# Kernel tuning notes

Measured on AMD Instinct MI355X. Metric: run time of the kernel, lower is better.

Reference implementation:

```python
import jax, jax.numpy as jnp
import numpy as np

BS = 1024
IN_DIM = 16 * 16      # final_dim[0]*final_dim[1]
HIDDEN = 3000
ITEM = 3              # item_number
STEPS = 30


def setup_inputs() -> dict:
    key = jax.random.key(0)
    ks = jax.random.split(key, 16)

    def xavier(k, shape):
        fan_in, fan_out = shape[1], shape[0]
        lim = np.sqrt(6.0 / (fan_in + fan_out))
        return jax.random.uniform(k, shape, jnp.float32, -lim, lim)

    return {
        "z": jax.random.normal(ks[0], (BS, 16, 16), jnp.float32),
        # join MLP: in->512->256->3000, ReLU after each
        "W1": xavier(ks[1], (512, IN_DIM)), "b1": jnp.zeros((512,), jnp.float32),
        "W2": xavier(ks[2], (256, 512)),    "b2": jnp.zeros((256,), jnp.float32),
        "W3": xavier(ks[3], (HIDDEN, 256)), "b3": jnp.zeros((HIDDEN,), jnp.float32),
        # GRUCell (torch layout: rows ordered r, z, n)
        "Wih": xavier(ks[4], (3 * HIDDEN, ITEM)),
        "bih": jnp.zeros((3 * HIDDEN,), jnp.float32),
        "Whh": xavier(ks[5], (3 * HIDDEN, HIDDEN)),
        "bhh": jnp.zeros((3 * HIDDEN,), jnp.float32),
        # output readout hidden -> item_number
        "Wo": xavier(ks[6], (ITEM, HIDDEN)), "bo": jnp.zeros((ITEM,), jnp.float32),
    }


def reference(z, W1, b1, W2, b2, W3, b3, Wih, bih, Whh, bhh, Wo, bo):
    bs = z.shape[0]
    zf = z.reshape(bs, -1)                                  # [bs, 256]
    h = jax.nn.relu(zf @ W1.T + b1)
    h = jax.nn.relu(h @ W2.T + b2)
    h = jax.nn.relu(h @ W3.T + b3)                          # [bs, 3000] initial hidden
    x0 = jnp.zeros((bs, ITEM), z.dtype)

    def step(carry, _):
        h, x = carry
        gi = x @ Wih.T + bih                                # [bs, 3H]
        gh = h @ Whh.T + bhh                                # [bs, 3H]
        i_r, i_z, i_n = jnp.split(gi, 3, axis=-1)
        h_r, h_z, h_n = jnp.split(gh, 3, axis=-1)
        r = jax.nn.sigmoid(i_r + h_r)
        u = jax.nn.sigmoid(i_z + h_z)
        n = jnp.tanh(i_n + r * h_n)
        h_new = (1.0 - u) * n + u * h
        x_new = h_new @ Wo.T + bo + x                       # residual waypoint add
        return (h_new, x_new), x_new

    (_, _), wp = jax.lax.scan(step, (h, x0), None, length=STEPS)
    return jnp.transpose(wp, (1, 0, 2))                      # [bs, STEPS, ITEM]
```

## Files before the change

kernel.cpp:

```cpp
#include <hip/hip_runtime.h>
#include <cstdint>
#include <cstddef>

#define HID 3000
#define HP  3072
#define NB  1024
#define BM  128
#define BN  64
#define KT  48
#define BUFSZ 53248

typedef _Float16 f16;
typedef _Float16 f16x8 __attribute__((ext_vector_type(8)));
typedef float    f32x4 __attribute__((ext_vector_type(4)));

__device__ __forceinline__ float sigf(float v)  { return 1.0f / (1.0f + __expf(-v)); }
__device__ __forceinline__ float tanhf_(float v){ return 2.0f / (1.0f + __expf(-2.0f * v)) - 1.0f; }

__device__ __forceinline__ void gload16(const void* g, void* l) {
    __builtin_amdgcn_global_load_lds((const __attribute__((address_space(1))) void*)g,
                                     (__attribute__((address_space(3))) void*)l, 16, 0, 0);
}

__global__ __launch_bounds__(256) void convert_whh(const float* __restrict__ whh,
                                                   f16* __restrict__ whh16)
{
    const int S32 = 3 * HP * (HP / 32);
    int t = blockIdx.x * 256 + threadIdx.x;
    if (t >= S32) return;
    const int c32 = (t % (HP / 32)) * 32;
    const int rr  = (t / (HP / 32)) % HP;
    const int g   = t / ((HP / 32) * HP);
    f16* dst = whh16 + ((size_t)g * HP + rr) * HP + c32;
    if (rr < HID && c32 + 32 <= HID) {
        const float* src = whh + (size_t)(g * HID + rr) * HID + c32;
#pragma unroll
        for (int u = 0; u < 4; ++u) {
            float4 lo = *reinterpret_cast<const float4*>(src + u * 8);
            float4 hi = *reinterpret_cast<const float4*>(src + u * 8 + 4);
            f16x8 v;
            v[0] = (f16)lo.x; v[1] = (f16)lo.y; v[2] = (f16)lo.z; v[3] = (f16)lo.w;
            v[4] = (f16)hi.x; v[5] = (f16)hi.y; v[6] = (f16)hi.z; v[7] = (f16)hi.w;
            *reinterpret_cast<f16x8*>(dst + u * 8) = v;
        }
    } else {
#pragma unroll
        for (int u = 0; u < 4; ++u) {
            f16x8 v;
#pragma unroll
            for (int k = 0; k < 8; ++k) {
                const int cc = c32 + u * 8 + k;
                v[k] = (rr < HID && cc < HID) ? (f16)whh[(size_t)(g * HID + rr) * HID + cc]
                                              : (f16)0.0f;
            }
            *reinterpret_cast<f16x8*>(dst + u * 8) = v;
        }
    }
}

__global__ __launch_bounds__(256) void convert_w3(const float* __restrict__ w,
                                                  f16* __restrict__ w16)
{
    int t = blockIdx.x * 256 + threadIdx.x;
    if (t >= HP * 32) return;
    int rr = t >> 5, c8 = (t & 31) * 8;
    f16x8 v;
    if (rr < HID) {
        const float* src = w + (size_t)rr * 256 + c8;
        float4 lo = *reinterpret_cast<const float4*>(src);
        float4 hi = *reinterpret_cast<const float4*>(src + 4);
        v[0] = (f16)lo.x; v[1] = (f16)lo.y; v[2] = (f16)lo.z; v[3] = (f16)lo.w;
        v[4] = (f16)hi.x; v[5] = (f16)hi.y; v[6] = (f16)hi.z; v[7] = (f16)hi.w;
    } else {
#pragma unroll
        for (int i = 0; i < 8; ++i) v[i] = (f16)0.0f;
    }
    *reinterpret_cast<f16x8*>(w16 + (size_t)rr * 256 + c8) = v;
}

__global__ __launch_bounds__(256) void mlp_layer(const float* __restrict__ A, int K, int N, int ldo,
                                                 const float* __restrict__ W,
                                                 const float* __restrict__ bias,
                                                 float* __restrict__ outf, f16* __restrict__ outh)
{
    __shared__ float sA[4 * 512];
    const int b0 = blockIdx.x * 4;
    for (int idx = threadIdx.x; idx < 4 * K; idx += 256)
        sA[idx] = A[(size_t)b0 * K + idx];
    __syncthreads();
    for (int n = threadIdx.x; n < ldo; n += 256) {
        float acc[4] = {0.f, 0.f, 0.f, 0.f};
        if (n < N) {
            const float4* wr = reinterpret_cast<const float4*>(W + (size_t)n * K);
            for (int kk = 0; kk < (K >> 2); ++kk) {
                float4 w = wr[kk];
#pragma unroll
                for (int r = 0; r < 4; ++r) {
                    const float* ar = sA + r * K + kk * 4;
                    acc[r] += ar[0] * w.x + ar[1] * w.y + ar[2] * w.z + ar[3] * w.w;
                }
            }
            float bv = bias[n];
#pragma unroll
            for (int r = 0; r < 4; ++r) acc[r] = fmaxf(acc[r] + bv, 0.f);
        }
#pragma unroll
        for (int r = 0; r < 4; ++r) {
            outf[(size_t)(b0 + r) * ldo + n] = acc[r];
            if (outh) outh[(size_t)(b0 + r) * ldo + n] = (f16)acc[r];
        }
    }
}

__global__ __launch_bounds__(256, 2)
void mlp3_mfma(const f16* __restrict__ A, const f16* __restrict__ B,
               const float* __restrict__ bias,
               float* __restrict__ outf, f16* __restrict__ outh)
{
    __shared__ __align__(16) char smem[24576];
    char* sBm = smem + 16384;

    const int tid  = threadIdx.x;
    const int lane = tid & 63;
    const int wid  = tid >> 6;
    const int wm = wid >> 1, wn = wid & 1;
    const int l15 = lane & 15, lhi = lane >> 4;
    const int swz = (lane & 7) << 4;

    const int gm0 = blockIdx.y * BM, gn0 = blockIdx.x * BN;

    const f16* a_srcs[4]; char* a_ldst[4];
#pragma unroll
    for (int i = 0; i < 4; ++i) {
        const int d = (i * 4 + wid) * 64 + lane;
        const int r = d >> 3;
        const int c = (d & 7) ^ (r & 7);
        a_srcs[i] = A + (size_t)(gm0 + r) * 256 + c * 8;
        a_ldst[i] = smem + (i * 4 + wid) * 1024;
    }
    const f16* b_srcs[2]; char* b_ldst[2];
#pragma unroll
    for (int i = 0; i < 2; ++i) {
        const int d = (i * 4 + wid) * 64 + lane;
        const int rr = d >> 3;
        const int c = (d & 7) ^ (rr & 7);
        b_srcs[i] = B + (size_t)(gn0 + rr) * 256 + c * 8;
        b_ldst[i] = sBm + (i * 4 + wid) * 1024;
    }

    f32x4 acc[4][2];
#pragma unroll
    for (int m = 0; m < 4; ++m)
#pragma unroll
        for (int n = 0; n < 2; ++n) acc[m][n] = (f32x4){0.f, 0.f, 0.f, 0.f};

    for (int kt = 0; kt < 4; ++kt) {
        const int kg = kt * 64;
#pragma unroll
        for (int i = 0; i < 4; ++i) gload16(a_srcs[i] + kg, a_ldst[i]);
#pragma unroll
        for (int i = 0; i < 2; ++i) gload16(b_srcs[i] + kg, b_ldst[i]);
        __syncthreads();
#pragma unroll
        for (int kk = 0; kk < 2; ++kk) {
            const int ko = (kk * 64 + lhi * 16) ^ swz;
            f16x8 af[4], bf[2];
#pragma unroll
            for (int m = 0; m < 4; ++m)
                af[m] = *reinterpret_cast<const f16x8*>(smem + (wm * 64 + m * 16 + l15) * 128 + ko);
#pragma unroll
            for (int n = 0; n < 2; ++n)
                bf[n] = *reinterpret_cast<const f16x8*>(sBm + (wn * 32 + n * 16 + l15) * 128 + ko);
#pragma unroll
            for (int m = 0; m < 4; ++m)
#pragma unroll
                for (int n = 0; n < 2; ++n)
                    acc[m][n] = __builtin_amdgcn_mfma_f32_16x16x32_f16(af[m], bf[n], acc[m][n], 0, 0, 0);
        }
        __syncthreads();
    }

#pragma unroll
    for (int m = 0; m < 4; ++m) {
#pragma unroll
        for (int e = 0; e < 4; ++e) {
            const int b = gm0 + wm * 64 + m * 16 + lhi * 4 + e;
#pragma unroll
            for (int n = 0; n < 2; ++n) {
                const int j = gn0 + wn * 32 + n * 16 + l15;
                if (j < HID) {
                    float v = fmaxf(acc[m][n][e] + bias[j], 0.f);
                    outf[(size_t)b * HP + j] = v;
                    outh[(size_t)b * HP + j] = (f16)v;
                }
            }
        }
    }
}

__global__ __launch_bounds__(256, 1)
void gru_step(const f16* __restrict__ h16c, float* __restrict__ hf32,
              const f16* __restrict__ whh16,
              const float* __restrict__ xprev,
              const float* __restrict__ Wih, const float* __restrict__ bih,
              const float* __restrict__ bhh,
              f16* __restrict__ h16n)
{
    __shared__ __align__(16) char smem[159744];

    const int tid  = threadIdx.x;
    const int lane = tid & 63;
    const int wid  = tid >> 6;
    const int wrow = (wid & 1) * 64;
    const int wcol = (wid >> 1) * 48;
    const int l15 = lane & 15, lhi = lane >> 4;
    const int swz = (lane & 7) << 4;

    const int id = blockIdx.x;
    const int xcd = id & 7, local = id >> 3;
    const int bn = xcd * 4 + (local & 3), bm = local >> 2;
    const int gm0 = bm * 128, gn0 = bn * 96;

    const f16* srcs[13];
#pragma unroll
    for (int i = 0; i < 4; ++i) {
        const int s = i * 256 + tid;
        const int r = s >> 3;
        const int c = (s & 7) ^ (r & 7);
        srcs[i] = h16c + (size_t)(gm0 + r) * HP + c * 8;
    }
#pragma unroll
    for (int i = 4; i < 13; ++i) {
        const int sb = (i - 4) * 256 + tid;
        const int rr = sb >> 3;
        const int g = rr / 96, jj = rr - g * 96;
        const int c = (sb & 7) ^ (rr & 7);
        srcs[i] = whh16 + (size_t)g * HP * HP + (size_t)(gn0 + jj) * HP + c * 8;
    }

    f32x4 acc[3][4][3];
#pragma unroll
    for (int g = 0; g < 3; ++g)
#pragma unroll
        for (int m = 0; m < 4; ++m)
#pragma unroll
            for (int n = 0; n < 3; ++n) acc[g][m][n] = (f32x4){0.f, 0.f, 0.f, 0.f};

    auto STAGE = [&](int kt, char* buf) {
        const int ko = kt * 64;
#pragma unroll
        for (int i = 0; i < 4; ++i)
            gload16(srcs[i] + ko, buf + i * 4096 + wid * 1024);
#pragma unroll
        for (int i = 4; i < 13; ++i)
            gload16(srcs[i] + ko, buf + 16384 + (i - 4) * 4096 + wid * 1024);
    };
    auto COMPUTE = [&](const char* buf) {
#pragma unroll
        for (int kk = 0; kk < 2; ++kk) {
            const int ko = (kk * 64 + lhi * 16) ^ swz;
            f16x8 af[4], bf[3][3];
#pragma unroll
            for (int m = 0; m < 4; ++m)
                af[m] = *reinterpret_cast<const f16x8*>(buf + (wrow + m * 16 + l15) * 128 + ko);
#pragma unroll
            for (int g = 0; g < 3; ++g)
#pragma unroll
                for (int n = 0; n < 3; ++n)
                    bf[g][n] = *reinterpret_cast<const f16x8*>(buf + 16384 + (g * 96 + wcol + n * 16 + l15) * 128 + ko);
            __builtin_amdgcn_s_setprio(1);
#pragma unroll
            for (int g = 0; g < 3; ++g)
#pragma unroll
                for (int m = 0; m < 4; ++m)
#pragma unroll
                    for (int n = 0; n < 3; ++n)
                        acc[g][m][n] = __builtin_amdgcn_mfma_f32_16x16x32_f16(af[m], bf[g][n], acc[g][m][n], 0, 0, 0);
            __builtin_amdgcn_s_setprio(0);
        }
    };

    STAGE(0, smem);
    STAGE(1, smem + BUFSZ);

    int cur = 0;
    for (int t = 0; t < KT; ++t) {
        if (t == KT - 1) asm volatile("s_waitcnt vmcnt(0)" ::: "memory");
        else             asm volatile("s_waitcnt vmcnt(13)" ::: "memory");
        __builtin_amdgcn_s_barrier();
        __builtin_amdgcn_sched_barrier(0);
        if (t + 2 < KT) {
            int b2 = cur + 2; if (b2 >= 3) b2 -= 3;
            STAGE(t + 2, smem + b2 * BUFSZ);
        }
        COMPUTE(smem + cur * BUFSZ);
        ++cur; if (cur == 3) cur = 0;
    }

#pragma unroll
    for (int m = 0; m < 4; ++m) {
#pragma unroll
        for (int e = 0; e < 4; ++e) {
            const int b = gm0 + wrow + m * 16 + lhi * 4 + e;
            const float x0 = xprev[b * 4 + 0], x1 = xprev[b * 4 + 1], x2 = xprev[b * 4 + 2];
#pragma unroll
            for (int n = 0; n < 3; ++n) {
                const int j = gn0 + wcol + n * 16 + l15;
                if (j < HID) {
                    const float g0 = acc[0][m][n][e];
                    const float g1 = acc[1][m][n][e];
                    const float g2 = acc[2][m][n][e];
                    const float* w0 = Wih + (size_t)j * 3;
                    const float* w1 = Wih + (size_t)(HID + j) * 3;
                    const float* w2 = Wih + (size_t)(2 * HID + j) * 3;
                    const float gi0 = x0 * w0[0] + x1 * w0[1] + x2 * w0[2] + bih[j];
                    const float gi1 = x0 * w1[0] + x1 * w1[1] + x2 * w1[2] + bih[HID + j];
                    const float gi2 = x0 * w2[0] + x1 * w2[1] + x2 * w2[2] + bih[2 * HID + j];
                    const float r = sigf(gi0 + g0 + bhh[j]);
                    const float u = sigf(gi1 + g1 + bhh[HID + j]);
                    const float nn = tanhf_(gi2 + r * (g2 + bhh[2 * HID + j]));
                    const float hp_ = hf32[(size_t)b * HP + j];
                    const float hn = (1.f - u) * nn + u * hp_;
                    hf32[(size_t)b * HP + j] = hn;
                    h16n[(size_t)b * HP + j] = (f16)hn;
                }
            }
        }
    }
}

__global__ __launch_bounds__(256) void x_update(const f16* __restrict__ hn,
                                                const float* __restrict__ Wo,
                                                const float* __restrict__ bo,
                                                const float* __restrict__ xp,
                                                float* __restrict__ xn,
                                                float* __restrict__ out, int s)
{
    const int b = blockIdx.x, tid = threadIdx.x;
    float a0 = 0.f, a1 = 0.f, a2 = 0.f;
    for (int ch = tid; ch < 375; ch += 256) {
        const int k = ch * 8;
        f16x8 h8 = *reinterpret_cast<const f16x8*>(hn + (size_t)b * HP + k);
#pragma unroll
        for (int i = 0; i < 8; ++i) {
            float hv = (float)h8[i];
            a0 += hv * Wo[k + i];
            a1 += hv * Wo[HID + k + i];
            a2 += hv * Wo[2 * HID + k + i];
        }
    }
#pragma unroll
    for (int off = 32; off; off >>= 1) {
        a0 += __shfl_down(a0, off);
        a1 += __shfl_down(a1, off);
        a2 += __shfl_down(a2, off);
    }
    __shared__ float red[3][4];
    const int lane = tid & 63, w = tid >> 6;
    if (lane == 0) { red[0][w] = a0; red[1][w] = a1; red[2][w] = a2; }
    __syncthreads();
    if (tid < 3) {
        float sres = red[tid][0] + red[tid][1] + red[tid][2] + red[tid][3];
        float xv = sres + bo[tid] + xp[b * 4 + tid];
        xn[b * 4 + tid] = xv;
        out[((size_t)b * 30 + s) * 3 + tid] = xv;
    }
}

extern "C" void kernel_launch(void* const* d_in, const int* in_sizes, int n_in,
                              void* d_out, int out_size, void* d_ws, size_t ws_size,
                              hipStream_t stream)
{
    (void)in_sizes; (void)n_in; (void)out_size; (void)ws_size;
    const float* z   = (const float*)d_in[0];
    const float* W1  = (const float*)d_in[1];
    const float* b1  = (const float*)d_in[2];
    const float* W2  = (const float*)d_in[3];
    const float* b2  = (const float*)d_in[4];
    const float* W3  = (const float*)d_in[5];
    const float* b3  = (const float*)d_in[6];
    const float* Wih = (const float*)d_in[7];
    const float* bih = (const float*)d_in[8];
    const float* Whh = (const float*)d_in[9];
    const float* bhh = (const float*)d_in[10];
    const float* Wo  = (const float*)d_in[11];
    const float* bo  = (const float*)d_in[12];
    float* out = (float*)d_out;

    char* ws = (char*)d_ws;
    size_t off = 0;
    f16* whh16 = (f16*)(ws + off); off += (size_t)3 * HP * HP * 2;
    f16* h16[2];
    h16[0] = (f16*)(ws + off); off += (size_t)NB * HP * 2;
    h16[1] = (f16*)(ws + off); off += (size_t)NB * HP * 2;
    float* hf  = (float*)(ws + off); off += (size_t)NB * HP * 4;
    float* h1  = (float*)(ws + off); off += (size_t)NB * 512 * 4;
    float* h2  = (float*)(ws + off); off += (size_t)NB * 256 * 4;
    f16*   h2h = (f16*)(ws + off);   off += (size_t)NB * 256 * 2;
    f16*   w3f16 = (f16*)(ws + off); off += (size_t)HP * 256 * 2;
    float* xb  = (float*)(ws + off); off += (size_t)31 * NB * 4 * 4;

    hipMemsetAsync(h16[0], 0, (size_t)2 * NB * HP * 2, stream);
    hipMemsetAsync(xb, 0, (size_t)NB * 4 * 4, stream);

    {
        int s32 = 3 * HP * (HP / 32);
        convert_whh<<<(s32 + 255) / 256, 256, 0, stream>>>(Whh, whh16);
    }
    convert_w3<<<(HP * 32 + 255) / 256, 256, 0, stream>>>(W3, w3f16);

    mlp_layer<<<NB / 4, 256, 0, stream>>>(z,  256, 512, 512, W1, b1, h1, nullptr);
    mlp_layer<<<NB / 4, 256, 0, stream>>>(h1, 512, 256, 256, W2, b2, h2, h2h);
    mlp3_mfma<<<dim3(HP / BN, NB / BM), 256, 0, stream>>>(h2h, w3f16, b3, hf, h16[0]);

    for (int s = 1; s <= 30; ++s) {
        int cur = (s - 1) & 1, nxt = s & 1;
        gru_step<<<256, 256, 0, stream>>>(
            h16[cur], hf, whh16, xb + (size_t)(s - 1) * NB * 4,
            Wih, bih, bhh, h16[nxt]);
        x_update<<<NB, 256, 0, stream>>>(h16[nxt], Wo, bo,
            xb + (size_t)(s - 1) * NB * 4, xb + (size_t)s * NB * 4, out, s - 1);
    }
}
```

Measured before the change: 2.636 ms.

## Split GRU GEMM K dimension across two wave sets with LDS reduction

Each gru_step block now runs 512 threads as two sets of four waves. Each set handles half of every K-tile (32 of 64 columns) in its own triple-buffered LDS region, using a new k-group-major LDS layout with no XOR swizzle. After the loop the two sets swap partial accumulators through LDS, and each finishes the gate epilogue for half of the rows. The goal is more waves per CU to hide latency and keep the MFMA units busy, at the cost of an extra cross-set reduction, two more barriers and smaller per-wave K-steps.

After: 6.310 ms. +139.4%, slower.

```diff
diff --git a/kernel.cpp b/kernel.cpp
--- a/kernel.cpp
+++ b/kernel.cpp
@@ -7,8 +7,9 @@
 #define NB  1024
 #define BM  128
 #define BN  64
-#define KT  48
-#define BUFSZ 53248
+#define NST 48
+#define SBUF 26624
+#define SETLDS 79872
 
 typedef _Float16 f16;
 typedef _Float16 f16x8 __attribute__((ext_vector_type(8)));
@@ -198,7 +199,7 @@
     }
 }
 
-__global__ __launch_bounds__(256, 1)
+__global__ __launch_bounds__(512, 2)
 void gru_step(const f16* __restrict__ h16c, float* __restrict__ hf32,
               const f16* __restrict__ whh16,
               const float* __restrict__ xprev,
@@ -211,32 +212,42 @@
     const int tid  = threadIdx.x;
     const int lane = tid & 63;
     const int wid  = tid >> 6;
-    const int wrow = (wid & 1) * 64;
-    const int wcol = (wid >> 1) * 48;
+    const int kset = wid >> 2;
+    const int ws   = wid & 3;
+    const int wrow = (ws & 1) * 64;
+    const int wcol = (ws >> 1) * 48;
     const int l15 = lane & 15, lhi = lane >> 4;
-    const int swz = (lane & 7) << 4;
+    const int u = ws * 64 + lane;
 
     const int id = blockIdx.x;
     const int xcd = id & 7, local = id >> 3;
     const int bn = xcd * 4 + (local & 3), bm = local >> 2;
     const int gm0 = bm * 128, gn0 = bn * 96;
 
-    const f16* srcs[13];
+    uint32_t offA[2], offB[5];
+#pragma unroll
+    for (int i = 0; i < 2; ++i) {
+        const int s = i * 256 + u;
+        const int kg = s >> 7, row = s & 127;
+        offA[i] = (uint32_t)(((gm0 + row) * HP + kg * 8) * 2) + (uint32_t)(kset * 3072);
+    }
 #pragma unroll
     for (int i = 0; i < 4; ++i) {
-        const int s = i * 256 + tid;
-        const int r = s >> 3;
-        const int c = (s & 7) ^ (r & 7);
-        srcs[i] = h16c + (size_t)(gm0 + r) * HP + c * 8;
-    }
-#pragma unroll
-    for (int i = 4; i < 13; ++i) {
-        const int sb = (i - 4) * 256 + tid;
-        const int rr = sb >> 3;
-        const int g = rr / 96, jj = rr - g * 96;
-        const int c = (sb & 7) ^ (rr & 7);
-        srcs[i] = whh16 + (size_t)g * HP * HP + (size_t)(gn0 + jj) * HP + c * 8;
-    }
+        const int sb = i * 256 + u;
+        const int kg = sb / 288, col = sb - kg * 288;
+        const int g = col / 96, jj = col - g * 96;
+        offB[i] = (uint32_t)(((size_t)g * HP * HP + (size_t)(gn0 + jj) * HP + kg * 8) * 2)
+                + (uint32_t)(kset * 3072);
+    }
+    {
+        const int sb = 1024 + (u & 127);
+        const int col = sb - 864;
+        const int g = col / 96, jj = col - g * 96;
+        offB[4] = (uint32_t)(((size_t)g * HP * HP + (size_t)(gn0 + jj) * HP + 3 * 8) * 2)
+                + (uint32_t)(kset * 3072);
+    }
+    const char* const h8 = (const char*)h16c;
+    const char* const w8 = (const char*)whh16;
 
     f32x4 acc[3][4][3];
 #pragma unroll
@@ -246,59 +257,94 @@
 #pragma unroll
             for (int n = 0; n < 3; ++n) acc[g][m][n] = (f32x4){0.f, 0.f, 0.f, 0.f};
 
-    auto STAGE = [&](int kt, char* buf) {
-        const int ko = kt * 64;
+    char* const setbase = smem + kset * SETLDS;
+
+    auto STAGE = [&](int t, char* buf) {
+        const uint32_t so = (uint32_t)(t * 64);
+#pragma unroll
+        for (int i = 0; i < 2; ++i)
+            gload16(h8 + offA[i] + so, buf + i * 4096 + ws * 1024);
 #pragma unroll
         for (int i = 0; i < 4; ++i)
-            gload16(srcs[i] + ko, buf + i * 4096 + wid * 1024);
-#pragma unroll
-        for (int i = 4; i < 13; ++i)
-            gload16(srcs[i] + ko, buf + 16384 + (i - 4) * 4096 + wid * 1024);
+            gload16(w8 + offB[i] + so, buf + 8192 + i * 4096 + ws * 1024);
+        if (ws < 2)
+            gload16(w8 + offB[4] + so, buf + 24576 + ws * 1024);
     };
     auto COMPUTE = [&](const char* buf) {
-#pragma unroll
-        for (int kk = 0; kk < 2; ++kk) {
-            const int ko = (kk * 64 + lhi * 16) ^ swz;
-            f16x8 af[4], bf[3][3];
+        const int ao = lhi * 2048 + (wrow + l15) * 16;
+        const int bo = 8192 + lhi * 4608 + (wcol + l15) * 16;
+        f16x8 af[4], bf[3][3];
+#pragma unroll
+        for (int m = 0; m < 4; ++m)
+            af[m] = *reinterpret_cast<const f16x8*>(buf + ao + m * 256);
+#pragma unroll
+        for (int g = 0; g < 3; ++g)
+#pragma unroll
+            for (int n = 0; n < 3; ++n)
+                bf[g][n] = *reinterpret_cast<const f16x8*>(buf + bo + g * 1536 + n * 256);
+        __builtin_amdgcn_s_setprio(1);
+#pragma unroll
+        for (int g = 0; g < 3; ++g)
 #pragma unroll
             for (int m = 0; m < 4; ++m)
-                af[m] = *reinterpret_cast<const f16x8*>(buf + (wrow + m * 16 + l15) * 128 + ko);
-#pragma unroll
-            for (int g = 0; g < 3; ++g)
 #pragma unroll
                 for (int n = 0; n < 3; ++n)
-                    bf[g][n] = *reinterpret_cast<const f16x8*>(buf + 16384 + (g * 96 + wcol + n * 16 + l15) * 128 + ko);
-            __builtin_amdgcn_s_setprio(1);
-#pragma unroll
-            for (int g = 0; g < 3; ++g)
-#pragma unroll
-                for (int m = 0; m < 4; ++m)
-#pragma unroll
-                    for (int n = 0; n < 3; ++n)
-                        acc[g][m][n] = __builtin_amdgcn_mfma_f32_16x16x32_f16(af[m], bf[g][n], acc[g][m][n], 0, 0, 0);
-            __builtin_amdgcn_s_setprio(0);
-        }
+                    acc[g][m][n] = __builtin_amdgcn_mfma_f32_16x16x32_f16(af[m], bf[g][n], acc[g][m][n], 0, 0, 0);
+        __builtin_amdgcn_s_setprio(0);
     };
 
-    STAGE(0, smem);
-    STAGE(1, smem + BUFSZ);
+    STAGE(0, setbase);
+    STAGE(1, setbase + SBUF);
 
     int cur = 0;
-    for (int t = 0; t < KT; ++t) {
-        if (t == KT - 1) asm volatile("s_waitcnt vmcnt(0)" ::: "memory");
-        else             asm volatile("s_waitcnt vmcnt(13)" ::: "memory");
+    for (int t = 0; t < NST; ++t) {
+        if (t == NST - 1)  asm volatile("s_waitcnt vmcnt(0)" ::: "memory");
+        else if (ws < 2)   asm volatile("s_waitcnt vmcnt(7)" ::: "memory");
+        else               asm volatile("s_waitcnt vmcnt(6)" ::: "memory");
         __builtin_amdgcn_s_barrier();
         __builtin_amdgcn_sched_barrier(0);
-        if (t + 2 < KT) {
+        if (t + 2 < NST) {
             int b2 = cur + 2; if (b2 >= 3) b2 -= 3;
-            STAGE(t + 2, smem + b2 * BUFSZ);
-        }
-        COMPUTE(smem + cur * BUFSZ);
+            STAGE(t + 2, setbase + b2 * SBUF);
+        }
+        COMPUTE(setbase + cur * SBUF);
         ++cur; if (cur == 3) cur = 0;
     }
 
-#pragma unroll
-    for (int m = 0; m < 4; ++m) {
+    __syncthreads();
+    {
+        char* wbase = smem + (kset ? 73728 : 0);
+        const int mgive = kset ? 0 : 2;
+#pragma unroll
+        for (int g = 0; g < 3; ++g)
+#pragma unroll
+            for (int mh = 0; mh < 2; ++mh)
+#pragma unroll
+                for (int n = 0; n < 3; ++n) {
+                    const int idx = (g * 2 + mh) * 3 + n;
+                    *reinterpret_cast<f32x4*>(wbase + ws * 18432 + idx * 1024 + lane * 16)
+                        = acc[g][mgive + mh][n];
+                }
+    }
+    __syncthreads();
+    const int mkeep = kset ? 2 : 0;
+    {
+        const char* rbase = smem + (kset ? 0 : 73728);
+#pragma unroll
+        for (int g = 0; g < 3; ++g)
+#pragma unroll
+            for (int mh = 0; mh < 2; ++mh)
+#pragma unroll
+                for (int n = 0; n < 3; ++n) {
+                    const int idx = (g * 2 + mh) * 3 + n;
+                    acc[g][mkeep + mh][n] +=
+                        *reinterpret_cast<const f32x4*>(rbase + ws * 18432 + idx * 1024 + lane * 16);
+                }
+    }
+
+#pragma unroll
+    for (int mh = 0; mh < 2; ++mh) {
+        const int m = mkeep + mh;
 #pragma unroll
         for (int e = 0; e < 4; ++e) {
             const int b = gm0 + wrow + m * 16 + lhi * 4 + e;
@@ -317,10 +363,10 @@
                     const float gi1 = x0 * w1[0] + x1 * w1[1] + x2 * w1[2] + bih[HID + j];
                     const float gi2 = x0 * w2[0] + x1 * w2[1] + x2 * w2[2] + bih[2 * HID + j];
                     const float r = sigf(gi0 + g0 + bhh[j]);
-                    const float u = sigf(gi1 + g1 + bhh[HID + j]);
+                    const float uu = sigf(gi1 + g1 + bhh[HID + j]);
                     const float nn = tanhf_(gi2 + r * (g2 + bhh[2 * HID + j]));
                     const float hp_ = hf32[(size_t)b * HP + j];
-                    const float hn = (1.f - u) * nn + u * hp_;
+                    const float hn = (1.f - uu) * nn + uu * hp_;
                     hf32[(size_t)b * HP + j] = hn;
                     h16n[(size_t)b * HP + j] = (f16)hn;
                 }
@@ -415,7 +461,7 @@
 
     for (int s = 1; s <= 30; ++s) {
         int cur = (s - 1) & 1, nxt = s & 1;
-        gru_step<<<256, 256, 0, stream>>>(
+        gru_step<<<256, 512, 0, stream>>>(
             h16[cur], hf, whh16, xb + (size_t)(s - 1) * NB * 4,
             Wih, bih, bhh, h16[nxt]);
         x_update<<<NB, 256, 0, stream>>>(h16[nxt], Wo, bo,
```

## Split GRU step tile across 12 waves with K-major LDS layout and two-phase staging

Applied to the files above, without the earlier changes.

Raises the GRU step block from 4 to 12 waves, so each wave owns a 32x32 sub-tile per gate instead of 64x48. Shared-memory staging switches from an XOR-swizzled row-major layout to a K-group-major layout. Each k-tile is split into two phases, each with its own partial global-to-LDS load and a barrier. The block-to-tile mapping is also changed so consecutive blocks vary along M. The aim is more latency hiding and less register pressure per wave, at the cost of extra barriers, a new wait-count scheme that must be exactly right, and possible LDS bank conflicts without the swizzle.

New measurement: 3.517 ms. 1.33x slower.

```diff
diff --git a/kernel.cpp b/kernel.cpp
--- a/kernel.cpp
+++ b/kernel.cpp
@@ -198,7 +198,7 @@
     }
 }
 
-__global__ __launch_bounds__(256, 1)
+__global__ __launch_bounds__(768, 3)
 void gru_step(const f16* __restrict__ h16c, float* __restrict__ hf32,
               const f16* __restrict__ whh16,
               const float* __restrict__ xprev,
@@ -211,101 +211,108 @@
     const int tid  = threadIdx.x;
     const int lane = tid & 63;
     const int wid  = tid >> 6;
-    const int wrow = (wid & 1) * 64;
-    const int wcol = (wid >> 1) * 48;
+    const int wm   = wid & 3;
+    const int wn   = wid >> 2;
     const int l15 = lane & 15, lhi = lane >> 4;
-    const int swz = (lane & 7) << 4;
 
     const int id = blockIdx.x;
     const int xcd = id & 7, local = id >> 3;
-    const int bn = xcd * 4 + (local & 3), bm = local >> 2;
+    const int bn = xcd * 4 + (local >> 3), bm = local & 7;
     const int gm0 = bm * 128, gn0 = bn * 96;
 
-    const f16* srcs[13];
-#pragma unroll
-    for (int i = 0; i < 4; ++i) {
-        const int s = i * 256 + tid;
-        const int r = s >> 3;
-        const int c = (s & 7) ^ (r & 7);
-        srcs[i] = h16c + (size_t)(gm0 + r) * HP + c * 8;
-    }
-#pragma unroll
-    for (int i = 4; i < 13; ++i) {
-        const int sb = (i - 4) * 256 + tid;
-        const int rr = sb >> 3;
-        const int g = rr / 96, jj = rr - g * 96;
-        const int c = (sb & 7) ^ (rr & 7);
-        srcs[i] = whh16 + (size_t)g * HP * HP + (size_t)(gn0 + jj) * HP + c * 8;
-    }
-
-    f32x4 acc[3][4][3];
+    const char* a_src0;
+    const char* a_src1 = nullptr;
+    const char* b_src[3];
+    {
+        const int s0 = tid;
+        a_src0 = (const char*)h16c + (size_t)((gm0 + (s0 & 127)) * HP + (s0 >> 7) * 8) * 2;
+        if (tid < 256) {
+            const int s1 = 768 + tid;
+            a_src1 = (const char*)h16c + (size_t)((gm0 + (s1 & 127)) * HP + (s1 >> 7) * 8) * 2;
+        }
+#pragma unroll
+        for (int i = 0; i < 3; ++i) {
+            const int sb = i * 768 + tid;
+            const int kg = sb / 288, col = sb - kg * 288;
+            const int g = col / 96, jj = col - g * 96;
+            b_src[i] = (const char*)whh16 +
+                       ((size_t)g * HP * HP + (size_t)(gn0 + jj) * HP + kg * 8) * 2;
+        }
+    }
+
+    f32x4 acc[3][2][2];
 #pragma unroll
     for (int g = 0; g < 3; ++g)
 #pragma unroll
-        for (int m = 0; m < 4; ++m)
-#pragma unroll
-            for (int n = 0; n < 3; ++n) acc[g][m][n] = (f32x4){0.f, 0.f, 0.f, 0.f};
-
-    auto STAGE = [&](int kt, char* buf) {
-        const int ko = kt * 64;
-#pragma unroll
-        for (int i = 0; i < 4; ++i)
-            gload16(srcs[i] + ko, buf + i * 4096 + wid * 1024);
-#pragma unroll
-        for (int i = 4; i < 13; ++i)
-            gload16(srcs[i] + ko, buf + 16384 + (i - 4) * 4096 + wid * 1024);
+        for (int m = 0; m < 2; ++m)
+#pragma unroll
+            for (int n = 0; n < 2; ++n) acc[g][m][n] = (f32x4){0.f, 0.f, 0.f, 0.f};
+
+    auto STAGE0 = [&](int t, char* buf) {
+        const uint32_t so = (uint32_t)t * 128u;
+        gload16(a_src0 + so, buf + tid * 16);
+        if (tid < 256) gload16(a_src1 + so, buf + (768 + tid) * 16);
+        gload16(b_src[0] + so, buf + 16384 + tid * 16);
     };
-    auto COMPUTE = [&](const char* buf) {
-#pragma unroll
-        for (int kk = 0; kk < 2; ++kk) {
-            const int ko = (kk * 64 + lhi * 16) ^ swz;
-            f16x8 af[4], bf[3][3];
-#pragma unroll
-            for (int m = 0; m < 4; ++m)
-                af[m] = *reinterpret_cast<const f16x8*>(buf + (wrow + m * 16 + l15) * 128 + ko);
-#pragma unroll
-            for (int g = 0; g < 3; ++g)
-#pragma unroll
-                for (int n = 0; n < 3; ++n)
-                    bf[g][n] = *reinterpret_cast<const f16x8*>(buf + 16384 + (g * 96 + wcol + n * 16 + l15) * 128 + ko);
-            __builtin_amdgcn_s_setprio(1);
-#pragma unroll
-            for (int g = 0; g < 3; ++g)
-#pragma unroll
-                for (int m = 0; m < 4; ++m)
-#pragma unroll
-                    for (int n = 0; n < 3; ++n)
-                        acc[g][m][n] = __builtin_amdgcn_mfma_f32_16x16x32_f16(af[m], bf[g][n], acc[g][m][n], 0, 0, 0);
-            __builtin_amdgcn_s_setprio(0);
-        }
+    auto STAGE1 = [&](int t, char* buf) {
+        const uint32_t so = (uint32_t)t * 128u;
+        gload16(b_src[1] + so, buf + 16384 + (768 + tid) * 16);
+        gload16(b_src[2] + so, buf + 16384 + (1536 + tid) * 16);
     };
 
-    STAGE(0, smem);
-    STAGE(1, smem + BUFSZ);
-
-    int cur = 0;
+    auto PHASE = [&](const char* buf, int kk) {
+        const int kg = kk * 4 + lhi;
+        const char* abase = buf + (kg * 128 + wm * 32 + l15) * 16;
+        const char* bbase = buf + 16384 + (kg * 288 + wn * 32 + l15) * 16;
+        f16x8 af[2], bf[3][2];
+#pragma unroll
+        for (int m = 0; m < 2; ++m)
+            af[m] = *reinterpret_cast<const f16x8*>(abase + m * 256);
+#pragma unroll
+        for (int g = 0; g < 3; ++g)
+#pragma unroll
+            for (int n = 0; n < 2; ++n)
+                bf[g][n] = *reinterpret_cast<const f16x8*>(bbase + (g * 96 + n * 16) * 16);
+        asm volatile("s_waitcnt lgkmcnt(0)" ::: "memory");
+        __builtin_amdgcn_sched_barrier(0);
+        __builtin_amdgcn_s_setprio(1);
+#pragma unroll
+        for (int g = 0; g < 3; ++g)
+#pragma unroll
+            for (int m = 0; m < 2; ++m)
+#pragma unroll
+                for (int n = 0; n < 2; ++n)
+                    acc[g][m][n] = __builtin_amdgcn_mfma_f32_16x16x32_f16(af[m], bf[g][n], acc[g][m][n], 0, 0, 0);
+        __builtin_amdgcn_s_setprio(0);
+    };
+
+    STAGE0(0, smem);            STAGE1(0, smem);
+    STAGE0(1, smem + BUFSZ);    STAGE1(1, smem + BUFSZ);
+
     for (int t = 0; t < KT; ++t) {
-        if (t == KT - 1) asm volatile("s_waitcnt vmcnt(0)" ::: "memory");
-        else             asm volatile("s_waitcnt vmcnt(13)" ::: "memory");
+        char* cbuf = smem + (t % 3) * BUFSZ;
+        char* nbuf = smem + ((t + 2) % 3) * BUFSZ;
+        if (t == KT - 1)  asm volatile("s_waitcnt vmcnt(0)" ::: "memory");
+        else if (wid < 4) asm volatile("s_waitcnt vmcnt(5)" ::: "memory");
+        else              asm volatile("s_waitcnt vmcnt(4)" ::: "memory");
         __builtin_amdgcn_s_barrier();
         __builtin_amdgcn_sched_barrier(0);
-        if (t + 2 < KT) {
-            int b2 = cur + 2; if (b2 >= 3) b2 -= 3;
-            STAGE(t + 2, smem + b2 * BUFSZ);
-        }
-        COMPUTE(smem + cur * BUFSZ);
-        ++cur; if (cur == 3) cur = 0;
-    }
-
-#pragma unroll
-    for (int m = 0; m < 4; ++m) {
+        if (t + 2 < KT) STAGE0(t + 2, nbuf);
+        PHASE(cbuf, 0);
+        __builtin_amdgcn_s_barrier();
+        if (t + 2 < KT) STAGE1(t + 2, nbuf);
+        PHASE(cbuf, 1);
+    }
+
+#pragma unroll
+    for (int m = 0; m < 2; ++m) {
 #pragma unroll
         for (int e = 0; e < 4; ++e) {
-            const int b = gm0 + wrow + m * 16 + lhi * 4 + e;
+            const int b = gm0 + wm * 32 + m * 16 + lhi * 4 + e;
             const float x0 = xprev[b * 4 + 0], x1 = xprev[b * 4 + 1], x2 = xprev[b * 4 + 2];
 #pragma unroll
-            for (int n = 0; n < 3; ++n) {
-                const int j = gn0 + wcol + n * 16 + l15;
+            for (int n = 0; n < 2; ++n) {
+                const int j = gn0 + wn * 32 + n * 16 + l15;
                 if (j < HID) {
                     const float g0 = acc[0][m][n][e];
                     const float g1 = acc[1][m][n][e];
@@ -415,7 +422,7 @@
 
     for (int s = 1; s <= 30; ++s) {
         int cur = (s - 1) & 1, nxt = s & 1;
-        gru_step<<<256, 256, 0, stream>>>(
+        gru_step<<<256, 768, 0, stream>>>(
             h16[cur], hf, whh16, xb + (size_t)(s - 1) * NB * 4,
             Wih, bih, bhh, h16[nxt]);
         x_update<<<NB, 256, 0, stream>>>(h16[nxt], Wo, bo,
```

## Retile GRU step GEMM into smaller, higher-occupancy blocks with thin K slabs

Applied to the files above, without the earlier changes.

The GRU recurrent GEMM moves from 256 blocks of 4 waves (128x96x3 tile, 64-wide K stages, about 156KB LDS) to 512 blocks of 6 waves (128x48x3 tile, 32-wide K slabs, about 51KB LDS). Launch bounds now allow three blocks per CU. The aim is more resident waves to hide memory latency and a simpler, swizzle-free LDS layout. In exchange, each wave issues fewer MFMAs between barriers, data reuse per tile is lower, and the h operand is reloaded from global memory by twice as many column blocks.

Result: slower. 4.380 ms (+66.2%).

```diff
diff --git a/kernel.cpp b/kernel.cpp
--- a/kernel.cpp
+++ b/kernel.cpp
@@ -7,8 +7,8 @@
 #define NB  1024
 #define BM  128
 #define BN  64
-#define KT  48
-#define BUFSZ 53248
+#define NSLAB 96
+#define SLAB 17408
 
 typedef _Float16 f16;
 typedef _Float16 f16x8 __attribute__((ext_vector_type(8)));
@@ -198,7 +198,7 @@
     }
 }
 
-__global__ __launch_bounds__(256, 1)
+__global__ __launch_bounds__(384, 3)
 void gru_step(const f16* __restrict__ h16c, float* __restrict__ hf32,
               const f16* __restrict__ whh16,
               const float* __restrict__ xprev,
@@ -206,124 +206,102 @@
               const float* __restrict__ bhh,
               f16* __restrict__ h16n)
 {
-    __shared__ __align__(16) char smem[159744];
+    __shared__ __align__(16) char smem[3 * SLAB];
 
     const int tid  = threadIdx.x;
     const int lane = tid & 63;
     const int wid  = tid >> 6;
-    const int wrow = (wid & 1) * 64;
-    const int wcol = (wid >> 1) * 48;
+    const int wm   = wid & 1;
+    const int wsub = wid >> 1;
     const int l15 = lane & 15, lhi = lane >> 4;
-    const int swz = (lane & 7) << 4;
 
     const int id = blockIdx.x;
     const int xcd = id & 7, local = id >> 3;
-    const int bn = xcd * 4 + (local & 3), bm = local >> 2;
-    const int gm0 = bm * 128, gn0 = bn * 96;
-
-    const f16* srcs[13];
-#pragma unroll
-    for (int i = 0; i < 4; ++i) {
-        const int s = i * 256 + tid;
-        const int r = s >> 3;
-        const int c = (s & 7) ^ (r & 7);
-        srcs[i] = h16c + (size_t)(gm0 + r) * HP + c * 8;
-    }
-#pragma unroll
-    for (int i = 4; i < 13; ++i) {
-        const int sb = (i - 4) * 256 + tid;
-        const int rr = sb >> 3;
-        const int g = rr / 96, jj = rr - g * 96;
-        const int c = (sb & 7) ^ (rr & 7);
-        srcs[i] = whh16 + (size_t)g * HP * HP + (size_t)(gn0 + jj) * HP + c * 8;
-    }
-
-    f32x4 acc[3][4][3];
+    const int bn = xcd * 8 + (local >> 3), bm = local & 7;
+    const int gm0 = bm * 128, gn0 = bn * 48;
+
+    const char* src[3];
+#pragma unroll
+    for (int i = 0; i < 3; ++i) {
+        const int s = i * 384 + tid;
+        if (s < 512) {
+            const int kg = s >> 7, row = s & 127;
+            src[i] = (const char*)(h16c + (size_t)(gm0 + row) * HP + kg * 8);
+        } else {
+            const int sb = (s - 512) % 576;
+            const int kg = sb / 144, col = sb - kg * 144;
+            const int g = col / 48, jj = col - g * 48;
+            src[i] = (const char*)(whh16 + (size_t)g * HP * HP + (size_t)(gn0 + jj) * HP + kg * 8);
+        }
+    }
+
+    f32x4 acc[3][4];
 #pragma unroll
     for (int g = 0; g < 3; ++g)
 #pragma unroll
-        for (int m = 0; m < 4; ++m)
-#pragma unroll
-            for (int n = 0; n < 3; ++n) acc[g][m][n] = (f32x4){0.f, 0.f, 0.f, 0.f};
-
-    auto STAGE = [&](int kt, char* buf) {
-        const int ko = kt * 64;
-#pragma unroll
-        for (int i = 0; i < 4; ++i)
-            gload16(srcs[i] + ko, buf + i * 4096 + wid * 1024);
-#pragma unroll
-        for (int i = 4; i < 13; ++i)
-            gload16(srcs[i] + ko, buf + 16384 + (i - 4) * 4096 + wid * 1024);
+        for (int m = 0; m < 4; ++m) acc[g][m] = (f32x4){0.f, 0.f, 0.f, 0.f};
+
+    auto STAGE = [&](int t, char* buf) {
+        const uint32_t so = (uint32_t)t * 64u;
+        gload16(src[0] + so, buf + tid * 16);
+        gload16(src[1] + so, buf + (384 + tid) * 16);
+        if (tid < 320) gload16(src[2] + so, buf + (768 + tid) * 16);
     };
     auto COMPUTE = [&](const char* buf) {
-#pragma unroll
-        for (int kk = 0; kk < 2; ++kk) {
-            const int ko = (kk * 64 + lhi * 16) ^ swz;
-            f16x8 af[4], bf[3][3];
+        const char* ab = buf + lhi * 2048 + (wm * 64 + l15) * 16;
+        const char* bb = buf + 8192 + lhi * 2304 + (wsub * 16 + l15) * 16;
+        f16x8 af[4], bf[3];
+#pragma unroll
+        for (int m = 0; m < 4; ++m)
+            af[m] = *reinterpret_cast<const f16x8*>(ab + m * 256);
+#pragma unroll
+        for (int g = 0; g < 3; ++g)
+            bf[g] = *reinterpret_cast<const f16x8*>(bb + g * 768);
+        __builtin_amdgcn_s_setprio(1);
+#pragma unroll
+        for (int g = 0; g < 3; ++g)
 #pragma unroll
             for (int m = 0; m < 4; ++m)
-                af[m] = *reinterpret_cast<const f16x8*>(buf + (wrow + m * 16 + l15) * 128 + ko);
-#pragma unroll
-            for (int g = 0; g < 3; ++g)
-#pragma unroll
-                for (int n = 0; n < 3; ++n)
-                    bf[g][n] = *reinterpret_cast<const f16x8*>(buf + 16384 + (g * 96 + wcol + n * 16 + l15) * 128 + ko);
-            __builtin_amdgcn_s_setprio(1);
-#pragma unroll
-            for (int g = 0; g < 3; ++g)
-#pragma unroll
-                for (int m = 0; m < 4; ++m)
-#pragma unroll
-                    for (int n = 0; n < 3; ++n)
-                        acc[g][m][n] = __builtin_amdgcn_mfma_f32_16x16x32_f16(af[m], bf[g][n], acc[g][m][n], 0, 0, 0);
-            __builtin_amdgcn_s_setprio(0);
-        }
+                acc[g][m] = __builtin_amdgcn_mfma_f32_16x16x32_f16(af[m], bf[g], acc[g][m], 0, 0, 0);
+        __builtin_amdgcn_s_setprio(0);
     };
 
     STAGE(0, smem);
-    STAGE(1, smem + BUFSZ);
-
-    int cur = 0;
-    for (int t = 0; t < KT; ++t) {
-        if (t == KT - 1) asm volatile("s_waitcnt vmcnt(0)" ::: "memory");
-        else             asm volatile("s_waitcnt vmcnt(13)" ::: "memory");
+    STAGE(1, smem + SLAB);
+
+    for (int t = 0; t < NSLAB; ++t) {
+        if (t == NSLAB - 1) asm volatile("s_waitcnt vmcnt(0)" ::: "memory");
+        else if (wid < 5)   asm volatile("s_waitcnt vmcnt(3)" ::: "memory");
+        else                asm volatile("s_waitcnt vmcnt(2)" ::: "memory");
         __builtin_amdgcn_s_barrier();
         __builtin_amdgcn_sched_barrier(0);
-        if (t + 2 < KT) {
-            int b2 = cur + 2; if (b2 >= 3) b2 -= 3;
-            STAGE(t + 2, smem + b2 * BUFSZ);
-        }
-        COMPUTE(smem + cur * BUFSZ);
-        ++cur; if (cur == 3) cur = 0;
-    }
-
-#pragma unroll
-    for (int m = 0; m < 4; ++m) {
-#pragma unroll
-        for (int e = 0; e < 4; ++e) {
-            const int b = gm0 + wrow + m * 16 + lhi * 4 + e;
-            const float x0 = xprev[b * 4 + 0], x1 = xprev[b * 4 + 1], x2 = xprev[b * 4 + 2];
-#pragma unroll
-            for (int n = 0; n < 3; ++n) {
-                const int j = gn0 + wcol + n * 16 + l15;
-                if (j < HID) {
-                    const float g0 = acc[0][m][n][e];
-                    const float g1 = acc[1][m][n][e];
-                    const float g2 = acc[2][m][n][e];
-                    const float* w0 = Wih + (size_t)j * 3;
-                    const float* w1 = Wih + (size_t)(HID + j) * 3;
-                    const float* w2 = Wih + (size_t)(2 * HID + j) * 3;
-                    const float gi0 = x0 * w0[0] + x1 * w0[1] + x2 * w0[2] + bih[j];
-                    const float gi1 = x0 * w1[0] + x1 * w1[1] + x2 * w1[2] + bih[HID + j];
-                    const float gi2 = x0 * w2[0] + x1 * w2[1] + x2 * w2[2] + bih[2 * HID + j];
-                    const float r = sigf(gi0 + g0 + bhh[j]);
-                    const float u = sigf(gi1 + g1 + bhh[HID + j]);
-                    const float nn = tanhf_(gi2 + r * (g2 + bhh[2 * HID + j]));
-                    const float hp_ = hf32[(size_t)b * HP + j];
-                    const float hn = (1.f - u) * nn + u * hp_;
-                    hf32[(size_t)b * HP + j] = hn;
-                    h16n[(size_t)b * HP + j] = (f16)hn;
-                }
+        if (t + 2 < NSLAB) STAGE(t + 2, smem + ((t + 2) % 3) * SLAB);
+        COMPUTE(smem + (t % 3) * SLAB);
+    }
+
+    const int j = gn0 + wsub * 16 + l15;
+    if (j < HID) {
+        const float* w0 = Wih + (size_t)j * 3;
+        const float* w1 = Wih + (size_t)(HID + j) * 3;
+        const float* w2 = Wih + (size_t)(2 * HID + j) * 3;
+        const float bi0 = bih[j] + bhh[j];
+        const float bi1 = bih[HID + j] + bhh[HID + j];
+        const float bi2 = bih[2 * HID + j];
+        const float bh2 = bhh[2 * HID + j];
+#pragma unroll
+        for (int m = 0; m < 4; ++m) {
+#pragma unroll
+            for (int e = 0; e < 4; ++e) {
+                const int b = gm0 + wm * 64 + m * 16 + lhi * 4 + e;
+                const float x0 = xprev[b * 4 + 0], x1 = xprev[b * 4 + 1], x2 = xprev[b * 4 + 2];
+                const float r = sigf(x0 * w0[0] + x1 * w0[1] + x2 * w0[2] + bi0 + acc[0][m][e]);
+                const float u = sigf(x0 * w1[0] + x1 * w1[1] + x2 * w1[2] + bi1 + acc[1][m][e]);
+                const float nn = tanhf_(x0 * w2[0] + x1 * w2[1] + x2 * w2[2] + bi2
+                                        + r * (acc[2][m][e] + bh2));
+                const float hp_ = hf32[(size_t)b * HP + j];
+                const float hn = (1.f - u) * nn + u * hp_;
+                hf32[(size_t)b * HP + j] = hn;
+                h16n[(size_t)b * HP + j] = (f16)hn;
             }
         }
     }
@@ -415,7 +393,7 @@
 
     for (int s = 1; s <= 30; ++s) {
         int cur = (s - 1) & 1, nxt = s & 1;
-        gru_step<<<256, 256, 0, stream>>>(
+        gru_step<<<512, 384, 0, stream>>>(
             h16[cur], hf, whh16, xb + (size_t)(s - 1) * NB * 4,
             Wih, bih, bhh, h16[nxt]);
         x_update<<<NB, 256, 0, stream>>>(h16[nxt], Wo, bo,
```
